# Kernel optimization log

Hardware: AMD Instinct MI355X
Metric: run time of the kernel (lower is better)

## Reference

```python
import jax, jax.numpy as jnp
import numpy as np

DIM = 64   # model dim == d_inner (expand=1)
Hh = 64
Ww = 64
BATCH = 4
D_IN = 64
N_ST = 8   # d_state
DT_R = 4   # dt_rank = ceil(dim/16)
K = 4      # depthwise conv kernel
NB = 8     # total CrossMambaBlocks: 4 (depth=1) + 4 final cross blocks


def setup_inputs():
    key = jax.random.key(0)
    ks = iter(jax.random.split(key, 40))
    def rn(shape, s=0.02):
        return jax.random.normal(next(ks), shape, jnp.float32) * s
    A_init = jnp.log(jnp.tile(jnp.arange(1, N_ST + 1, dtype=jnp.float32), (NB, D_IN, 1)))
    return dict(
        img1=rn((BATCH, DIM, Hh, Ww), 1.0), img2=rn((BATCH, DIM, Hh, Ww), 1.0),
        img1_sum=rn((BATCH, DIM, Hh, Ww), 1.0), img2_sum=rn((BATCH, DIM, Hh, Ww), 1.0),
        norm0_w=jnp.ones((NB, DIM)), norm0_b=jnp.zeros((NB, DIM)),
        norm1_w=jnp.ones((NB, DIM)), norm1_b=jnp.zeros((NB, DIM)),
        in_w=rn((NB, 2 * D_IN, DIM)), in_b=jnp.zeros((NB, 2 * D_IN)),
        conv_w_f=rn((NB, D_IN, 1, K), 0.1), conv_b_f=jnp.zeros((NB, D_IN)),
        conv_w_b=rn((NB, D_IN, 1, K), 0.1), conv_b_b=jnp.zeros((NB, D_IN)),
        xproj_w_f=rn((NB, DT_R + 2 * N_ST, D_IN)), xproj_w_b=rn((NB, DT_R + 2 * N_ST, D_IN)),
        dtproj_w_f=rn((NB, D_IN, DT_R), 0.1), dtproj_b_f=jnp.zeros((NB, D_IN)),
        dtproj_w_b=rn((NB, D_IN, DT_R), 0.1), dtproj_b_b=jnp.zeros((NB, D_IN)),
        A_log_f=A_init, A_log_b=A_init,
        D_f=jnp.ones((NB, D_IN)), D_b=jnp.ones((NB, D_IN)),
        ln_w=jnp.ones((NB, D_IN)), ln_b=jnp.zeros((NB, D_IN)),
        mout_w=rn((NB, DIM, D_IN)), mout_b=jnp.zeros((NB, DIM)),
        fop_w=rn((DIM, 2 * DIM)), fop_b=jnp.zeros((DIM,)),
    )


def _ln(x, w, b):
    m = x.mean(-1, keepdims=True)
    v = ((x - m) ** 2).mean(-1, keepdims=True)
    return (x - m) * jax.lax.rsqrt(v + 1e-5) * w + b


def _dwconv(x, w, b):
    # x: [b,L,d], w: [d,1,K] depthwise causal conv along L
    y = jax.lax.conv_general_dilated(
        x.transpose(0, 2, 1), w, (1,), [(K - 1, 0)],
        dimension_numbers=('NCH', 'OIH', 'NCH'),
        feature_group_count=x.shape[-1])
    return y.transpose(0, 2, 1) + b


def _ssm(u, dt, Bm, Cm, A, Dm):
    # u,dt: [b,L,d]; Bm,Cm: [b,L,n]; A: [d,n]; Dm: [d]
    dA = jnp.exp(dt[..., None] * A)                 # [b,L,d,n]
    dBu = (dt * u)[..., None] * Bm[:, :, None, :]   # [b,L,d,n]
    def step(h, xs):
        dA_t, dBu_t, C_t = xs
        h = dA_t * h + dBu_t
        return h, jnp.einsum('bdn,bn->bd', h, C_t)
    h0 = jnp.zeros(u.shape[:1] + A.shape, u.dtype)
    _, ys = jax.lax.scan(step, h0, (jnp.moveaxis(dA, 1, 0), jnp.moveaxis(dBu, 1, 0), jnp.moveaxis(Cm, 1, 0)))
    return jnp.moveaxis(ys, 0, 1) + u * Dm


def _direction(x_in, extra, conv_w, conv_b, xproj_w, dtproj_w, dtproj_b, A_log, Dm, flip):
    if flip:
        x_in = x_in[:, ::-1]
        extra = extra[:, ::-1]
    u = jax.nn.silu(_dwconv(x_in, conv_w, conv_b))
    dbl = jnp.einsum('bld,ed->ble', extra, xproj_w)     # cross: dt/B/C from extra embedding
    dtr = dbl[..., :DT_R]
    Bm = dbl[..., DT_R:DT_R + N_ST]
    Cm = dbl[..., DT_R + N_ST:]
    dt = jax.nn.softplus(jnp.einsum('blr,dr->bld', dtr, dtproj_w) + dtproj_b)
    y = _ssm(u, dt, Bm, Cm, -jnp.exp(A_log), Dm)
    if flip:
        y = y[:, ::-1]
    return y


def _cross_block(i, x, extra, p):
    skip = x
    x = _ln(x, p['norm0_w'][i], p['norm0_b'][i])
    extra = _ln(extra, p['norm1_w'][i], p['norm1_b'][i])
    xz = jnp.einsum('bld,ed->ble', x, p['in_w'][i]) + p['in_b'][i]
    x_in, z = xz[..., :D_IN], xz[..., D_IN:]
    y_f = _direction(x_in, extra, p['conv_w_f'][i], p['conv_b_f'][i], p['xproj_w_f'][i],
                     p['dtproj_w_f'][i], p['dtproj_b_f'][i], p['A_log_f'][i], p['D_f'][i], False)
    y_b = _direction(x_in, extra, p['conv_w_b'][i], p['conv_b_b'][i], p['xproj_w_b'][i],
                     p['dtproj_w_b'][i], p['dtproj_b_b'][i], p['A_log_b'][i], p['D_b'][i], True)
    y = 0.5 * (y_f + y_b)                    # if_devide_out=True
    y = _ln(y, p['ln_w'][i], p['ln_b'][i])   # use_norm=True
    y = y * jax.nn.silu(z)
    out = jnp.einsum('bld,ed->ble', y, p['mout_w'][i]) + p['mout_b'][i]
    return out + skip


def _forward(img1, img2, img1_sum, img2_sum, norm0_w, norm0_b, norm1_w, norm1_b, in_w, in_b,
             conv_w_f, conv_b_f, conv_w_b, conv_b_b, xproj_w_f, xproj_w_b,
             dtproj_w_f, dtproj_b_f, dtproj_w_b, dtproj_b_b, A_log_f, A_log_b,
             D_f, D_b, ln_w, ln_b, mout_w, mout_b, fop_w, fop_b):
    p = dict(norm0_w=norm0_w, norm0_b=norm0_b, norm1_w=norm1_w, norm1_b=norm1_b,
             in_w=in_w, in_b=in_b, conv_w_f=conv_w_f, conv_b_f=conv_b_f,
             conv_w_b=conv_w_b, conv_b_b=conv_b_b, xproj_w_f=xproj_w_f, xproj_w_b=xproj_w_b,
             dtproj_w_f=dtproj_w_f, dtproj_b_f=dtproj_b_f, dtproj_w_b=dtproj_w_b,
             dtproj_b_b=dtproj_b_b, A_log_f=A_log_f, A_log_b=A_log_b, D_f=D_f, D_b=D_b,
             ln_w=ln_w, ln_b=ln_b, mout_w=mout_w, mout_b=mout_b)
    def seq(t):
        b, c, h, w = t.shape
        return t.reshape(b, c, h * w).transpose(0, 2, 1)   # b (h w) c
    s1, s2, s1s, s2s = seq(img1), seq(img2), seq(img1_sum), seq(img2_sum)
    # depth=1 cross-fusion loop
    s1 = _cross_block(0, s1, s1s, p)
    s2 = _cross_block(1, s2, s2s, p)
    s1s = _cross_block(2, s1s, s1, p)
    s2s = _cross_block(3, s2s, s2, p)
    # final cross blocks
    i1l = _cross_block(4, s1, s2, p)
    i1g = _cross_block(5, s1, s2s, p)
    i2l = _cross_block(6, s2, s1, p)
    i2g = _cross_block(7, s2, s1s, p)
    c1 = jnp.concatenate([i1l, i1g], -1)
    c2 = jnp.concatenate([i2l, i2g], -1)
    fusion = jnp.einsum('ble,ce->blc', 0.5 * (c1 + c2), fop_w) + fop_b
    b = img1.shape[0]
    return fusion.transpose(0, 2, 1).reshape(b, DIM, Hh, Ww)


def reference(img1, img2, img1_sum, img2_sum, norm0_w, norm0_b, norm1_w, norm1_b, in_w, in_b,
              conv_w_f, conv_b_f, conv_w_b, conv_b_b, xproj_w_f, xproj_w_b,
              dtproj_w_f, dtproj_b_f, dtproj_w_b, dtproj_b_b, A_log_f, A_log_b,
              D_f, D_b, ln_w, ln_b, mout_w, mout_b, fop_w, fop_b):
    return _forward(img1, img2, img1_sum, img2_sum, norm0_w, norm0_b, norm1_w, norm1_b, in_w, in_b,
                    conv_w_f, conv_b_f, conv_w_b, conv_b_b, xproj_w_f, xproj_w_b,
                    dtproj_w_f, dtproj_b_f, dtproj_w_b, dtproj_b_b, A_log_f, A_log_b,
                    D_f, D_b, ln_w, ln_b, mout_w, mout_b, fop_w, fop_b)
```

## Files before the change

### kernel.cpp

```cpp
#include <hip/hip_runtime.h>
#include <hip/hip_bf16.h>

#define BX 4
#define LX 4096
#define DX 64
#define NX 8
#define TCH 16
#define NCH 256
#define BLD (BX*LX*DX)

typedef unsigned short u16;
typedef __attribute__((ext_vector_type(8))) short v8s;
typedef __attribute__((ext_vector_type(4))) float v4f;

#define L2E 1.44269504088896f
#define LN2 0.69314718055994531f

__device__ __forceinline__ float b2f(u16 u){ return __uint_as_float(((unsigned)u)<<16); }
__device__ __forceinline__ u16 f2b(float f){
  unsigned u = __float_as_uint(f);
  unsigned r = (u + 0x7FFFu + ((u>>16)&1u)) >> 16;
  return (u16)r;
}
__device__ __forceinline__ float siluf(float x){
  return x * __builtin_amdgcn_rcpf(1.f + __builtin_amdgcn_exp2f(-x*L2E));
}
__device__ __forceinline__ float softplusf(float x){
  const float t = __builtin_amdgcn_exp2f(-fabsf(x)*L2E);
  return fmaxf(x, 0.f) + LN2 * __builtin_amdgcn_logf(1.f + t);
}

__device__ __forceinline__ v4f mfma16(v8s a, v8s b, v4f c){
  return __builtin_amdgcn_mfma_f32_16x16x32_bf16(a, b, c, 0, 0, 0);
}
__device__ __forceinline__ void split8(const float* v, v8s& hi, v8s& lo){
  #pragma unroll
  for(int j=0;j<8;j++){
    const short h = (short)f2b(v[j]);
    hi[j] = h;
    lo[j] = (short)f2b(v[j] - b2f((u16)h));
  }
}
__device__ __forceinline__ void afrag(const float* tile, int lane, int k0, v8s& hi, v8s& lo){
  const float* p = tile + (lane&15)*72 + k0 + ((lane>>4)<<3);
  float v[8];
  const float4 a = *(const float4*)(p);
  const float4 b = *(const float4*)(p+4);
  v[0]=a.x; v[1]=a.y; v[2]=a.z; v[3]=a.w;
  v[4]=b.x; v[5]=b.y; v[6]=b.z; v[7]=b.w;
  split8(v, hi, lo);
}

struct Ctx {
  const float *nw0,*nb0,*nw1,*nb1;
  const float *inw,*inb;
  const float *convw,*convb;
  const float *xproj;
  const float *dtw,*dtb;
  const float *A2,*Dp;
  const float *lnw,*lnb;
  const float *moutw,*moutb;
  const float *fopw,*fopb;
  const u16 *wih,*wil,*wxh,*wxl,*wmh,*wml,*wfh,*wfl;
  float *act[4], *outc[4];
  float *xin[4], *zz[4], *dbl[4], *yy[4], *Pp[4], *qq[4], *hin[4];
};

struct BlkDesc { int i; const float* x; const float* e; float* out; int slot; };
struct StageArgs { BlkDesc d[4]; };

struct PrepEnt { const void* src; float* dst; int n; int mode; };
struct PrepAll { PrepEnt a[26]; };

__global__ __launch_bounds__(256) void k_prep(PrepAll pa, const u16* df){
  const bool isbf = (df[0] == 0x3F80u);
  PrepEnt p = pa.a[blockIdx.y];
  int idx = blockIdx.x*256 + threadIdx.x;
  if(idx < p.n){
    float v = isbf ? b2f(((const u16*)p.src)[idx]) : ((const float*)p.src)[idx];
    if(p.mode==2) v = -__expf(v) * L2E;
    p.dst[idx] = v;
  }
}

struct WPrep { const float* src; u16* dh; u16* dl; int E; int KS; int kind; int i; };
struct WPrepAll { WPrep a[25]; };

__global__ __launch_bounds__(64) void k_prepw(WPrepAll wa, const float* xprojbase){
  WPrep p = wa.a[blockIdx.y];
  const int NT = (p.E + 15) >> 4;
  const int idx = blockIdx.x;
  if(idx >= NT*p.KS) return;
  const int ct = idx / p.KS, ks = idx % p.KS;
  const int lane = threadIdx.x;
  const int g  = ct*16 + (lane & 15);
  const int k0 = ks*32 + ((lane>>4)<<3);
  const int K  = p.KS*32;
  bool valid; const float* srcp = nullptr;
  if(p.kind == 1){
    valid = (g < 40);
    if(valid){ const int dir = g/20, e = g - dir*20;
      srcp = xprojbase + ((size_t)(dir*8 + p.i)*20 + e)*64 + k0; }
  } else {
    valid = (g < p.E);
    if(valid) srcp = p.src + (size_t)g*K + k0;
  }
  float v[8];
  #pragma unroll
  for(int j=0;j<8;j++) v[j] = valid ? srcp[j] : 0.f;
  v8s hi, lo; split8(v, hi, lo);
  const size_t o = ((size_t)idx*64 + lane)*8;
  *(v8s*)(p.dh + o) = hi;
  *(v8s*)(p.dl + o) = lo;
}

struct SeqArgs { const void* src[4]; };

__global__ __launch_bounds__(256) void k_seq(SeqArgs s, Ctx c, const u16* df){
  const bool isbf = (df[0] == 0x3F80u);
  __shared__ float ld[64*65];
  const int t = blockIdx.z, b = blockIdx.y, l0 = blockIdx.x*64;
  float* dst = c.act[t];
  const int tx = threadIdx.x, ty = threadIdx.y;
  if(isbf){
    const u16* src = (const u16*)s.src[t];
    #pragma unroll
    for(int k=0;k<16;k++){ int d = k*4+ty; ld[d*65+tx] = b2f(src[(size_t)(b*64+d)*LX + l0+tx]); }
  } else {
    const float* src = (const float*)s.src[t];
    #pragma unroll
    for(int k=0;k<16;k++){ int d = k*4+ty; ld[d*65+tx] = src[(size_t)(b*64+d)*LX + l0+tx]; }
  }
  __syncthreads();
  #pragma unroll
  for(int k=0;k<16;k++){ int p = k*4+ty; dst[(size_t)(b*LX + l0+p)*64 + tx] = ld[tx*65+p]; }
}

__device__ __forceinline__ void coop72(float* sb, const float* g, int t){
  #pragma unroll
  for(int k=0;k<4;k++){
    const int idx = k*256 + t;
    const int row = idx >> 4;
    const int c4  = (idx & 15) << 2;
    *(float4*)(sb + row*72 + c4) = *(const float4*)(g + (size_t)row*64 + c4);
  }
}
__device__ __forceinline__ void coop72_avg(float* sb, const float* g0, const float* g1, int t){
  #pragma unroll
  for(int k=0;k<4;k++){
    const int idx = k*256 + t;
    const int row = idx >> 4;
    const int c4  = (idx & 15) << 2;
    const float4 a = *(const float4*)(g0 + (size_t)row*64 + c4);
    const float4 b = *(const float4*)(g1 + (size_t)row*64 + c4);
    float4 o; o.x=0.5f*(a.x+b.x); o.y=0.5f*(a.y+b.y); o.z=0.5f*(a.z+b.z); o.w=0.5f*(a.w+b.w);
    *(float4*)(sb + row*72 + c4) = o;
  }
}

__device__ __forceinline__ void ln72(float* sb, int lane, const float* w, const float* b){
  float r[64];
  float* p = sb + lane*72;
  #pragma unroll
  for(int cc=0;cc<64;cc+=4){ float4 v = *(const float4*)(p+cc); r[cc]=v.x; r[cc+1]=v.y; r[cc+2]=v.z; r[cc+3]=v.w; }
  float m=0.f;
  #pragma unroll
  for(int d=0;d<64;d++) m += r[d];
  m *= (1.f/64.f);
  float va=0.f;
  #pragma unroll
  for(int d=0;d<64;d++){ float t=r[d]-m; va += t*t; }
  va *= (1.f/64.f);
  const float rs = rsqrtf(va + 1e-5f);
  #pragma unroll
  for(int d=0;d<64;d++) r[d] = (r[d]-m)*rs*w[d] + b[d];
  #pragma unroll
  for(int cc=0;cc<64;cc+=4){ float4 v={r[cc],r[cc+1],r[cc+2],r[cc+3]}; *(float4*)(p+cc)=v; }
}

__global__ __launch_bounds__(256) void k_front(Ctx c, StageArgs sa){
  __shared__ __align__(16) float sx[64*72];
  __shared__ __align__(16) float se[64*72];
  const BlkDesc bd = sa.d[blockIdx.y];
  const int i = bd.i;
  const int tile = blockIdx.x;
  const int b = tile >> 6;
  const int l0 = (tile & 63) << 6;
  const int bl0 = b*LX + l0;
  const int t = threadIdx.x;
  const int wave = t >> 6, lane = t & 63;

  coop72(sx, bd.x + (size_t)bl0*64, t);
  coop72(se, bd.e + (size_t)bl0*64, t);
  __syncthreads();
  if(wave == 0)      ln72(sx, lane, c.nw0 + i*64, c.nb0 + i*64);
  else if(wave == 1) ln72(se, lane, c.nw1 + i*64, c.nb1 + i*64);
  __syncthreads();

  const int m0 = wave*16;
  const int q  = lane >> 4;
  const int n15 = lane & 15;

  {
    v8s ah[2], al[2];
    afrag(sx + m0*72, lane, 0,  ah[0], al[0]);
    afrag(sx + m0*72, lane, 32, ah[1], al[1]);
    const v8s* WH = (const v8s*)c.wih + (size_t)i*1024;
    const v8s* WL = (const v8s*)c.wil + (size_t)i*1024;
    #pragma unroll 1
    for(int ct=0; ct<8; ct++){
      const int colg = ct*16 + n15;
      const float bias = c.inb[i*128 + colg];
      v4f acc = {bias, bias, bias, bias};
      #pragma unroll
      for(int ks=0; ks<2; ks++){
        const v8s wh = WH[(ct*2+ks)*64 + lane];
        const v8s wl = WL[(ct*2+ks)*64 + lane];
        acc = mfma16(ah[ks], wl, acc);
        acc = mfma16(al[ks], wh, acc);
        acc = mfma16(ah[ks], wh, acc);
      }
      float* baseo = (colg < 64) ? c.xin[bd.slot] : c.zz[bd.slot];
      const int col = colg & 63;
      #pragma unroll
      for(int r=0;r<4;r++){
        const int row = m0 + q*4 + r;
        baseo[(size_t)(bl0+row)*64 + col] = acc[r];
      }
    }
  }
  {
    v8s ah[2], al[2];
    afrag(se + m0*72, lane, 0,  ah[0], al[0]);
    afrag(se + m0*72, lane, 32, ah[1], al[1]);
    const v8s* WH = (const v8s*)c.wxh + (size_t)i*384;
    const v8s* WL = (const v8s*)c.wxl + (size_t)i*384;
    #pragma unroll 1
    for(int ct=0; ct<3; ct++){
      v4f acc = {0.f,0.f,0.f,0.f};
      #pragma unroll
      for(int ks=0; ks<2; ks++){
        const v8s wh = WH[(ct*2+ks)*64 + lane];
        const v8s wl = WL[(ct*2+ks)*64 + lane];
        acc = mfma16(ah[ks], wl, acc);
        acc = mfma16(al[ks], wh, acc);
        acc = mfma16(ah[ks], wh, acc);
      }
      const int g = ct*16 + n15;
      if(g < 40){
        const int dir = (g >= 20);
        const int e = g - dir*20;
        float* dp = c.dbl[bd.slot] + (size_t)dir*((size_t)BX*LX*20);
        #pragma unroll
        for(int r=0;r<4;r++){
          const int row = m0 + q*4 + r;
          dp[(size_t)(bl0+row)*20 + e] = acc[r];
        }
      }
    }
  }
}

template<int PASS>
__device__ __forceinline__ void scan_body(const Ctx& c, const StageArgs& sa){
  __shared__ float meta[TCH*20];
  const int zid = blockIdx.z;
  const int j = zid >> 1, dir = zid & 1;
  const BlkDesc bd = sa.d[j];
  const int i = bd.i, slot = bd.slot;
  const int ch = blockIdx.x, b = blockIdx.y;
  const int d = threadIdx.x;
  const int pb = (dir*8 + i)*64 + d;

  const float4 cwv = *(const float4*)(c.convw + (size_t)pb*4);
  const float  cbv = c.convb[pb];
  const float4 dwv = *(const float4*)(c.dtw + (size_t)pb*4);
  const float  dtbv = c.dtb[pb];
  const float4 A2a = *(const float4*)(c.A2 + (size_t)pb*8);
  const float4 A2b = *(const float4*)(c.A2 + (size_t)pb*8 + 4);
  float A2[8] = {A2a.x,A2a.y,A2a.z,A2a.w,A2b.x,A2b.y,A2b.z,A2b.w};

  {
    const float4* s = (const float4*)(c.dbl[slot] + (size_t)dir*((size_t)BX*LX*20)
                                      + (size_t)(b*LX + ch*TCH)*20);
    float4* dst = (float4*)meta;
    #pragma unroll
    for(int k=0;k<2;k++){ int idx = k*64 + d; if(idx < 80) dst[idx] = s[idx]; }
  }
  __syncthreads();

  const float* X = c.xin[slot] + (size_t)b*LX*64 + d;
  float h[8];
  if(PASS==1){
    #pragma unroll
    for(int n=0;n<8;n++) h[n]=0.f;
  } else {
    const float* hp = c.hin[slot] + (size_t)(dir*NCH + ch)*((size_t)BX*512) + (size_t)b*512 + d;
    #pragma unroll
    for(int n=0;n<8;n++) h[n] = hp[n*64];
  }
  const float Dv = (PASS==3) ? c.Dp[pb] : 0.f;
  float* Y = (PASS==3) ? (c.yy[slot] + (size_t)(dir*BX + b)*LX*64 + d) : (float*)0;

  int lbase, sgn;
  if(dir==0){ lbase = ch*TCH;          sgn =  1; }
  else      { lbase = ch*TCH + TCH-1;  sgn = -1; }
  float w0,w1,w2;
  { int p0 = lbase - 3*sgn; w0 = (p0>=0 && p0<LX)? X[(size_t)p0*64] : 0.f; }
  { int p1 = lbase - 2*sgn; w1 = (p1>=0 && p1<LX)? X[(size_t)p1*64] : 0.f; }
  { int p2 = lbase - 1*sgn; w2 = (p2>=0 && p2<LX)? X[(size_t)p2*64] : 0.f; }

  const float* Xp = X + (size_t)lbase*64;
  float* Yp = (PASS==3) ? (Y + (size_t)lbase*64) : (float*)0;
  const float* mp = meta + (dir ? (TCH-1)*20 : 0);
  const int xstep = sgn*64;
  const int mstep = sgn*20;

  float S = 0.f;
  #pragma unroll 4
  for(int t=0;t<TCH;t++){
    const float xc = *Xp;
    const float u = siluf(cwv.x*w0 + cwv.y*w1 + cwv.z*w2 + cwv.w*xc + cbv);
    const float4 m0  = *(const float4*)(mp);
    const float4 mb0 = *(const float4*)(mp+4);
    const float4 mb1 = *(const float4*)(mp+8);
    const float dt = softplusf(m0.x*dwv.x + m0.y*dwv.y + m0.z*dwv.z + m0.w*dwv.w + dtbv);
    const float du = dt*u;
    const float Bv[8] = {mb0.x,mb0.y,mb0.z,mb0.w,mb1.x,mb1.y,mb1.z,mb1.w};
    #pragma unroll
    for(int n=0;n<8;n++){
      const float dA = __builtin_amdgcn_exp2f(dt*A2[n]);
      h[n] = dA*h[n] + du*Bv[n];
    }
    if(PASS==3){
      const float4 mc0 = *(const float4*)(mp+12);
      const float4 mc1 = *(const float4*)(mp+16);
      const float Cv[8] = {mc0.x,mc0.y,mc0.z,mc0.w,mc1.x,mc1.y,mc1.z,mc1.w};
      float yv = u*Dv;
      #pragma unroll
      for(int n=0;n<8;n++) yv += h[n]*Cv[n];
      *Yp = yv;
      Yp += xstep;
    } else {
      S += dt;
    }
    w0=w1; w1=w2; w2=xc;
    Xp += xstep; mp += mstep;
  }
  if(PASS==1){
    float* Pw = c.Pp[slot] + (size_t)(dir*NCH + ch)*((size_t)BX*512) + (size_t)b*512 + d;
    float* Qw = c.qq[slot] + (size_t)(dir*NCH + ch)*((size_t)BX*512) + (size_t)b*512 + d;
    #pragma unroll
    for(int n=0;n<8;n++){
      Pw[n*64] = __builtin_amdgcn_exp2f(A2[n]*S);
      Qw[n*64] = h[n];
    }
  }
}

__global__ __launch_bounds__(64) void k_scan1(Ctx c, StageArgs sa){ scan_body<1>(c, sa); }
__global__ __launch_bounds__(64) void k_scan3(Ctx c, StageArgs sa){ scan_body<3>(c, sa); }

__global__ __launch_bounds__(64) void k_mid(Ctx c, StageArgs sa){
  const int b = blockIdx.x >> 3;
  const int seg = blockIdx.x & 7;
  const int dir = blockIdx.y & 1, j = blockIdx.y >> 1;
  const BlkDesc bd = sa.d[j];
  const int slot = bd.slot;
  const int nd = seg*64 + threadIdx.x;
  const size_t base = (size_t)dir*NCH*((size_t)BX*512) + (size_t)b*512 + nd;
  const size_t STR = (size_t)BX*512;
  const float* P = c.Pp[slot] + base;
  const float* Q = c.qq[slot] + base;
  float* H = c.hin[slot] + base;
  float h = 0.f;
  float Pv[16], Qv[16];
  #pragma unroll 1
  for(int g=0; g<NCH/16; g++){
    #pragma unroll
    for(int k=0;k<16;k++){
      const int ch = dir ? (NCH-1 - (g*16+k)) : (g*16+k);
      Pv[k] = P[(size_t)ch*STR]; Qv[k] = Q[(size_t)ch*STR];
    }
    #pragma unroll
    for(int k=0;k<16;k++){
      const int ch = dir ? (NCH-1 - (g*16+k)) : (g*16+k);
      H[(size_t)ch*STR] = h;
      h = fmaf(Pv[k], h, Qv[k]);
    }
  }
}

__global__ __launch_bounds__(256) void k_back(Ctx c, StageArgs sa){
  __shared__ __align__(16) float sy[64*72];
  __shared__ __align__(16) float sz[64*72];
  __shared__ __align__(16) float sk[64*72];
  const BlkDesc bd = sa.d[blockIdx.y];
  const int i = bd.i, slot = bd.slot;
  const int tile = blockIdx.x;
  const int b = tile >> 6;
  const int l0 = (tile & 63) << 6;
  const int bl0 = b*LX + l0;
  const int t = threadIdx.x;
  const int wave = t >> 6, lane = t & 63;

  coop72_avg(sy, c.yy[slot] + (size_t)b*LX*64 + (size_t)l0*64,
                 c.yy[slot] + (size_t)(BX+b)*LX*64 + (size_t)l0*64, t);
  coop72(sz, c.zz[slot] + (size_t)bl0*64, t);
  coop72(sk, bd.x + (size_t)bl0*64, t);
  __syncthreads();
  if(wave == 0){
    ln72(sy, lane, c.lnw + i*64, c.lnb + i*64);
    float* p = sy + lane*72;
    const float* zp = sz + lane*72;
    #pragma unroll
    for(int d=0;d<64;d++){ const float zv = zp[d]; p[d] *= siluf(zv)/(zv==0.f?1.f:zv)*zv; }
  }
  __syncthreads();

  const int m0 = wave*16;
  const int q  = lane >> 4;
  const int n15 = lane & 15;
  v8s ah[2], al[2];
  afrag(sy + m0*72, lane, 0,  ah[0], al[0]);
  afrag(sy + m0*72, lane, 32, ah[1], al[1]);
  const v8s* WH = (const v8s*)c.wmh + (size_t)i*512;
  const v8s* WL = (const v8s*)c.wml + (size_t)i*512;
  #pragma unroll 1
  for(int ct=0; ct<4; ct++){
    const int col = ct*16 + n15;
    const float bias = c.moutb[i*64 + col];
    v4f acc = {bias, bias, bias, bias};
    #pragma unroll
    for(int ks=0; ks<2; ks++){
      const v8s wh = WH[(ct*2+ks)*64 + lane];
      const v8s wl = WL[(ct*2+ks)*64 + lane];
      acc = mfma16(ah[ks], wl, acc);
      acc = mfma16(al[ks], wh, acc);
      acc = mfma16(ah[ks], wh, acc);
    }
    #pragma unroll
    for(int r=0;r<4;r++){
      const int row = m0 + q*4 + r;
      bd.out[(size_t)(bl0+row)*64 + col] = acc[r] + sk[row*72 + col];
    }
  }
}

__global__ __launch_bounds__(256) void k_fusion(Ctx c, void* outp, const u16* df){
  const bool isbf = (df[0] == 0x3F80u);
  __shared__ __align__(16) float sL[64*72];
  __shared__ __align__(16) float sH[64*72];
  __shared__ __align__(16) float sT[64*68];
  const int tile = blockIdx.x;
  const int b = tile >> 6;
  const int l0 = (tile & 63) << 6;
  const int bl0 = b*LX + l0;
  const int t = threadIdx.x;
  const int wave = t >> 6, lane = t & 63;

  coop72_avg(sL, c.outc[0] + (size_t)bl0*64, c.outc[2] + (size_t)bl0*64, t);
  coop72_avg(sH, c.outc[1] + (size_t)bl0*64, c.outc[3] + (size_t)bl0*64, t);
  __syncthreads();

  const int m0 = wave*16;
  const int q  = lane >> 4;
  const int n15 = lane & 15;
  v8s ah[4], al[4];
  afrag(sL + m0*72, lane, 0,  ah[0], al[0]);
  afrag(sL + m0*72, lane, 32, ah[1], al[1]);
  afrag(sH + m0*72, lane, 0,  ah[2], al[2]);
  afrag(sH + m0*72, lane, 32, ah[3], al[3]);
  const v8s* WH = (const v8s*)c.wfh;
  const v8s* WL = (const v8s*)c.wfl;
  #pragma unroll 1
  for(int ct=0; ct<4; ct++){
    const int col = ct*16 + n15;
    const float bias = c.fopb[col];
    v4f acc = {bias, bias, bias, bias};
    #pragma unroll
    for(int ks=0; ks<4; ks++){
      const v8s wh = WH[(ct*4+ks)*64 + lane];
      const v8s wl = WL[(ct*4+ks)*64 + lane];
      acc = mfma16(ah[ks], wl, acc);
      acc = mfma16(al[ks], wh, acc);
      acc = mfma16(ah[ks], wh, acc);
    }
    #pragma unroll
    for(int r=0;r<4;r++) sT[col*68 + m0 + q*4 + r] = acc[r];
  }
  __syncthreads();

  const int o  = t >> 2;
  const int p0 = (t & 3) * 16;
  float v[16];
  #pragma unroll
  for(int k=0;k<16;k+=4){
    const float4 x = *(const float4*)(sT + o*68 + p0 + k);
    v[k]=x.x; v[k+1]=x.y; v[k+2]=x.z; v[k+3]=x.w;
  }
  const size_t off = (size_t)(b*64+o)*LX + l0 + p0;
  if(isbf){
    u16 hb[16];
    #pragma unroll
    for(int k=0;k<16;k++) hb[k] = f2b(v[k]);
    uint4 u0, u1;
    u0.x = hb[0] | ((unsigned)hb[1]<<16);  u0.y = hb[2] | ((unsigned)hb[3]<<16);
    u0.z = hb[4] | ((unsigned)hb[5]<<16);  u0.w = hb[6] | ((unsigned)hb[7]<<16);
    u1.x = hb[8] | ((unsigned)hb[9]<<16);  u1.y = hb[10]| ((unsigned)hb[11]<<16);
    u1.z = hb[12]| ((unsigned)hb[13]<<16); u1.w = hb[14]| ((unsigned)hb[15]<<16);
    *(uint4*)((u16*)outp + off)     = u0;
    *(uint4*)((u16*)outp + off + 8) = u1;
  } else {
    float* fo = (float*)outp + off;
    #pragma unroll
    for(int k=0;k<16;k+=4){ float4 x={v[k],v[k+1],v[k+2],v[k+3]}; *(float4*)(fo+k)=x; }
  }
}

extern "C" void kernel_launch(void* const* d_in, const int* in_sizes, int n_in,
                              void* d_out, int out_size, void* d_ws, size_t ws_size,
                              hipStream_t stream){
  (void)in_sizes; (void)out_size;
  if(n_in < 30) return;
  const u16* df = (const u16*)d_in[22];
  float* w = (float*)d_ws;
  size_t off = 0;
  auto al = [&](size_t n){ float* p = w + off; off += n; return p; };

  Ctx c;
  float* nw0 = al(512);  float* nb0 = al(512);
  float* nw1 = al(512);  float* nb1 = al(512);
  float* inw = al(65536); float* inb = al(1024);
  float* convw = al(4096); float* convb = al(1024);
  float* xproj = al(20480);
  float* dtw = al(4096); float* dtb = al(1024);
  float* A2 = al(8192);  float* Dp = al(1024);
  float* lnw = al(512);  float* lnb = al(512);
  float* moutw = al(32768); float* moutb = al(512);
  float* fopw = al(8192); float* fopb = al(64);
  c.nw0=nw0; c.nb0=nb0; c.nw1=nw1; c.nb1=nb1;
  c.inw=inw; c.inb=inb; c.convw=convw; c.convb=convb;
  c.xproj=xproj; c.dtw=dtw; c.dtb=dtb; c.A2=A2; c.Dp=Dp;
  c.lnw=lnw; c.lnb=lnb; c.moutw=moutw; c.moutb=moutb; c.fopw=fopw; c.fopb=fopb;

  u16* wih = (u16*)al(32768); u16* wil = (u16*)al(32768);
  u16* wxh = (u16*)al(12288); u16* wxl = (u16*)al(12288);
  u16* wmh = (u16*)al(16384); u16* wml = (u16*)al(16384);
  u16* wfh = (u16*)al(4096);  u16* wfl = (u16*)al(4096);
  c.wih=wih; c.wil=wil; c.wxh=wxh; c.wxl=wxl; c.wmh=wmh; c.wml=wml; c.wfh=wfh; c.wfl=wfl;

  for(int k=0;k<4;k++) c.act[k]  = al(BLD);
  for(int k=0;k<4;k++) c.outc[k] = al(BLD);

  const size_t CHW = 2*(size_t)NCH*BX*512;
  const size_t SLOT = (size_t)BLD + BLD + 2*(size_t)BX*LX*20 + 2*(size_t)BLD + 3*CHW;
  const size_t avail = ws_size/4;
  int nslots = 4;
  while(nslots>1 && off + (size_t)nslots*SLOT > avail) nslots >>= 1;
  for(int s=0;s<nslots;s++){
    c.xin[s]=al(BLD); c.zz[s]=al(BLD); c.dbl[s]=al(2*(size_t)BX*LX*20);
    c.yy[s]=al(2*(size_t)BLD);
    c.Pp[s]=al(CHW); c.qq[s]=al(CHW); c.hin[s]=al(CHW);
  }
  for(int s=nslots;s<4;s++){
    c.xin[s]=c.xin[0]; c.zz[s]=c.zz[0]; c.dbl[s]=c.dbl[0]; c.yy[s]=c.yy[0];
    c.Pp[s]=c.Pp[0]; c.qq[s]=c.qq[0]; c.hin[s]=c.hin[0];
  }

  PrepAll pa;
  int kk = 0;
  auto add = [&](int idx, float* dst, int n, int mode){
    pa.a[kk].src=d_in[idx]; pa.a[kk].dst=dst; pa.a[kk].n=n; pa.a[kk].mode=mode; kk++;
  };
  add(4,  nw0, 512, 0); add(5,  nb0, 512, 0);
  add(6,  nw1, 512, 0); add(7,  nb1, 512, 0);
  add(8,  inw, 65536, 0); add(9, inb, 1024, 0);
  add(10, convw, 2048, 0);      add(11, convb, 512, 0);
  add(12, convw+2048, 2048, 0); add(13, convb+512, 512, 0);
  add(14, xproj, 10240, 0);     add(15, xproj+10240, 10240, 0);
  add(16, dtw, 2048, 0);        add(17, dtb, 512, 0);
  add(18, dtw+2048, 2048, 0);   add(19, dtb+512, 512, 0);
  add(20, A2, 4096, 2);         add(21, A2+4096, 4096, 2);
  add(22, Dp, 512, 0);          add(23, Dp+512, 512, 0);
  add(24, lnw, 512, 0);         add(25, lnb, 512, 0);
  add(26, moutw, 32768, 0);     add(27, moutb, 512, 0);
  add(28, fopw, 8192, 0);       add(29, fopb, 64, 0);
  k_prep<<<dim3(256,26),256,0,stream>>>(pa, df);

  WPrepAll wa;
  for(int i=0;i<8;i++) wa.a[i]    = { inw + (size_t)i*8192,  wih + (size_t)i*8192, wil + (size_t)i*8192, 128, 2, 0, i };
  for(int i=0;i<8;i++) wa.a[8+i]  = { nullptr,               wxh + (size_t)i*3072, wxl + (size_t)i*3072,  48, 2, 1, i };
  for(int i=0;i<8;i++) wa.a[16+i] = { moutw + (size_t)i*4096, wmh + (size_t)i*4096, wml + (size_t)i*4096, 64, 2, 0, i };
  wa.a[24] = { fopw, wfh, wfl, 64, 4, 0, 0 };
  k_prepw<<<dim3(16,25),64,0,stream>>>(wa, xproj);

  SeqArgs sq;
  for(int t=0;t<4;t++) sq.src[t] = d_in[t];
  k_seq<<<dim3(64,BX,4), dim3(64,4), 0, stream>>>(sq, c, df);

  BlkDesc SA[2] = {{0, c.act[0], c.act[2], c.act[0], 0},
                   {1, c.act[1], c.act[3], c.act[1], 0}};
  BlkDesc SB[2] = {{2, c.act[2], c.act[0], c.act[2], 0},
                   {3, c.act[3], c.act[1], c.act[3], 0}};
  BlkDesc SC[4] = {{4, c.act[0], c.act[1], c.outc[0], 0},
                   {5, c.act[0], c.act[3], c.outc[1], 0},
                   {6, c.act[1], c.act[0], c.outc[2], 0},
                   {7, c.act[1], c.act[2], c.outc[3], 0}};

  auto run = [&](BlkDesc* ds, int cnt){
    for(int k=0;k<cnt;k+=nslots){
      int n = cnt-k; if(n>nslots) n = nslots;
      StageArgs sa;
      for(int j=0;j<n;j++){ sa.d[j] = ds[k+j]; sa.d[j].slot = j; }
      for(int j=n;j<4;j++) sa.d[j] = sa.d[0];
      k_front<<<dim3(256,n),      256, 0, stream>>>(c, sa);
      k_scan1<<<dim3(NCH,BX,2*n),  64, 0, stream>>>(c, sa);
      k_mid  <<<dim3(BX*8,2*n),    64, 0, stream>>>(c, sa);
      k_scan3<<<dim3(NCH,BX,2*n),  64, 0, stream>>>(c, sa);
      k_back <<<dim3(256,n),      256, 0, stream>>>(c, sa);
    }
  };
  run(SA,2); run(SB,2); run(SC,4);
  k_fusion<<<256,256,0,stream>>>(c, d_out, df);
}
```

Baseline: 387.1 us.

## Merge weight prep kernels, rebalance block stages, widen mid-scan unroll, simplify gating

The scalar-parameter conversion and the hi/lo bf16 weight splitting now run in a single launch. The split now reads the original inputs directly, so the intermediate fp32 copies of the in, x-proj, out and fusion weights are no longer made. The block schedule is regrouped so two of the final cross blocks run alongside blocks 2 and 3, giving stages of 2, 4 and 2 blocks. The mid-chunk carry scan loads 32 chunks per batch instead of 16, and the SiLU gating expression is reduced to a plain multiply. Together these aim to cut launch count, prep traffic and some per-element arithmetic. The cost is a more complex prep kernel and higher register use in the mid scan.

```diff
diff --git a/kernel.cpp b/kernel.cpp
--- a/kernel.cpp
+++ b/kernel.cpp
@@ -53,14 +53,13 @@
 
 struct Ctx {
   const float *nw0,*nb0,*nw1,*nb1;
-  const float *inw,*inb;
+  const float *inb;
   const float *convw,*convb;
-  const float *xproj;
   const float *dtw,*dtb;
   const float *A2,*Dp;
   const float *lnw,*lnb;
-  const float *moutw,*moutb;
-  const float *fopw,*fopb;
+  const float *moutb;
+  const float *fopb;
   const u16 *wih,*wil,*wxh,*wxl,*wmh,*wml,*wfh,*wfl;
   float *act[4], *outc[4];
   float *xin[4], *zz[4], *dbl[4], *yy[4], *Pp[4], *qq[4], *hin[4];
@@ -70,48 +69,52 @@
 struct StageArgs { BlkDesc d[4]; };
 
 struct PrepEnt { const void* src; float* dst; int n; int mode; };
-struct PrepAll { PrepEnt a[26]; };
-
-__global__ __launch_bounds__(256) void k_prep(PrepAll pa, const u16* df){
+struct PrepAll { PrepEnt a[21]; };
+struct WPrep { const void* sA; const void* sB; u16* dh; u16* dl; long off; int E; int KS; int kind; int i; };
+struct WPrepAll { WPrep a[25]; };
+
+__global__ __launch_bounds__(256) void k_prep(PrepAll pa, WPrepAll wa, const u16* df){
   const bool isbf = (df[0] == 0x3F80u);
-  PrepEnt p = pa.a[blockIdx.y];
-  int idx = blockIdx.x*256 + threadIdx.x;
-  if(idx < p.n){
-    float v = isbf ? b2f(((const u16*)p.src)[idx]) : ((const float*)p.src)[idx];
-    if(p.mode==2) v = -__expf(v) * L2E;
-    p.dst[idx] = v;
-  }
-}
-
-struct WPrep { const float* src; u16* dh; u16* dl; int E; int KS; int kind; int i; };
-struct WPrepAll { WPrep a[25]; };
-
-__global__ __launch_bounds__(64) void k_prepw(WPrepAll wa, const float* xprojbase){
-  WPrep p = wa.a[blockIdx.y];
-  const int NT = (p.E + 15) >> 4;
-  const int idx = blockIdx.x;
-  if(idx >= NT*p.KS) return;
-  const int ct = idx / p.KS, ks = idx % p.KS;
-  const int lane = threadIdx.x;
-  const int g  = ct*16 + (lane & 15);
-  const int k0 = ks*32 + ((lane>>4)<<3);
-  const int K  = p.KS*32;
-  bool valid; const float* srcp = nullptr;
-  if(p.kind == 1){
-    valid = (g < 40);
-    if(valid){ const int dir = g/20, e = g - dir*20;
-      srcp = xprojbase + ((size_t)(dir*8 + p.i)*20 + e)*64 + k0; }
+  if(blockIdx.y < 21){
+    PrepEnt p = pa.a[blockIdx.y];
+    int idx = blockIdx.x*256 + threadIdx.x;
+    if(idx < p.n){
+      float v = isbf ? b2f(((const u16*)p.src)[idx]) : ((const float*)p.src)[idx];
+      if(p.mode==2) v = -__expf(v) * L2E;
+      p.dst[idx] = v;
+    }
   } else {
-    valid = (g < p.E);
-    if(valid) srcp = p.src + (size_t)g*K + k0;
-  }
-  float v[8];
-  #pragma unroll
-  for(int j=0;j<8;j++) v[j] = valid ? srcp[j] : 0.f;
-  v8s hi, lo; split8(v, hi, lo);
-  const size_t o = ((size_t)idx*64 + lane)*8;
-  *(v8s*)(p.dh + o) = hi;
-  *(v8s*)(p.dl + o) = lo;
+    WPrep p = wa.a[blockIdx.y - 21];
+    const int wv = threadIdx.x >> 6, lane = threadIdx.x & 63;
+    const int idx = blockIdx.x*4 + wv;
+    const int NT = (p.E + 15) >> 4;
+    if(idx >= NT*p.KS) return;
+    const int ct = idx / p.KS, ks = idx % p.KS;
+    const int g  = ct*16 + (lane & 15);
+    const int k0 = ks*32 + ((lane>>4)<<3);
+    const int K  = p.KS*32;
+    bool valid; long si = 0; const void* sp = p.sA;
+    if(p.kind == 1){
+      valid = (g < 40);
+      const int dir = g/20, e = g - dir*20;
+      if(dir) sp = p.sB;
+      si = ((long)p.i*20 + e)*64 + k0;
+    } else {
+      valid = (g < p.E);
+      si = p.off + (long)g*K + k0;
+    }
+    float v[8];
+    #pragma unroll
+    for(int j2=0;j2<8;j2++){
+      float x = 0.f;
+      if(valid) x = isbf ? b2f(((const u16*)sp)[si+j2]) : ((const float*)sp)[si+j2];
+      v[j2] = x;
+    }
+    v8s hi, lo; split8(v, hi, lo);
+    const size_t o = ((size_t)idx*64 + lane)*8;
+    *(v8s*)(p.dh + o) = hi;
+    *(v8s*)(p.dl + o) = lo;
+  }
 }
 
 struct SeqArgs { const void* src[4]; };
@@ -263,7 +266,7 @@
 
 template<int PASS>
 __device__ __forceinline__ void scan_body(const Ctx& c, const StageArgs& sa){
-  __shared__ float meta[TCH*20];
+  __shared__ __align__(16) float meta[TCH*20];
   const int zid = blockIdx.z;
   const int j = zid >> 1, dir = zid & 1;
   const BlkDesc bd = sa.d[j];
@@ -374,17 +377,17 @@
   const float* Q = c.qq[slot] + base;
   float* H = c.hin[slot] + base;
   float h = 0.f;
-  float Pv[16], Qv[16];
+  float Pv[32], Qv[32];
   #pragma unroll 1
-  for(int g=0; g<NCH/16; g++){
-    #pragma unroll
-    for(int k=0;k<16;k++){
-      const int ch = dir ? (NCH-1 - (g*16+k)) : (g*16+k);
+  for(int g=0; g<NCH/32; g++){
+    #pragma unroll
+    for(int k=0;k<32;k++){
+      const int ch = dir ? (NCH-1 - (g*32+k)) : (g*32+k);
       Pv[k] = P[(size_t)ch*STR]; Qv[k] = Q[(size_t)ch*STR];
     }
     #pragma unroll
-    for(int k=0;k<16;k++){
-      const int ch = dir ? (NCH-1 - (g*16+k)) : (g*16+k);
+    for(int k=0;k<32;k++){
+      const int ch = dir ? (NCH-1 - (g*32+k)) : (g*32+k);
       H[(size_t)ch*STR] = h;
       h = fmaf(Pv[k], h, Qv[k]);
     }
@@ -414,7 +417,7 @@
     float* p = sy + lane*72;
     const float* zp = sz + lane*72;
     #pragma unroll
-    for(int d=0;d<64;d++){ const float zv = zp[d]; p[d] *= siluf(zv)/(zv==0.f?1.f:zv)*zv; }
+    for(int d=0;d<64;d++){ p[d] *= siluf(zp[d]); }
   }
   __syncthreads();
 
@@ -531,18 +534,17 @@
   Ctx c;
   float* nw0 = al(512);  float* nb0 = al(512);
   float* nw1 = al(512);  float* nb1 = al(512);
-  float* inw = al(65536); float* inb = al(1024);
+  float* inb = al(1024);
   float* convw = al(4096); float* convb = al(1024);
-  float* xproj = al(20480);
   float* dtw = al(4096); float* dtb = al(1024);
   float* A2 = al(8192);  float* Dp = al(1024);
   float* lnw = al(512);  float* lnb = al(512);
-  float* moutw = al(32768); float* moutb = al(512);
-  float* fopw = al(8192); float* fopb = al(64);
+  float* moutb = al(512);
+  float* fopb = al(64);
   c.nw0=nw0; c.nb0=nb0; c.nw1=nw1; c.nb1=nb1;
-  c.inw=inw; c.inb=inb; c.convw=convw; c.convb=convb;
-  c.xproj=xproj; c.dtw=dtw; c.dtb=dtb; c.A2=A2; c.Dp=Dp;
-  c.lnw=lnw; c.lnb=lnb; c.moutw=moutw; c.moutb=moutb; c.fopw=fopw; c.fopb=fopb;
+  c.inb=inb; c.convw=convw; c.convb=convb;
+  c.dtw=dtw; c.dtb=dtb; c.A2=A2; c.Dp=Dp;
+  c.lnw=lnw; c.lnb=lnb; c.moutb=moutb; c.fopb=fopb;
 
   u16* wih = (u16*)al(32768); u16* wil = (u16*)al(32768);
   u16* wxh = (u16*)al(12288); u16* wxl = (u16*)al(12288);
@@ -575,37 +577,36 @@
   };
   add(4,  nw0, 512, 0); add(5,  nb0, 512, 0);
   add(6,  nw1, 512, 0); add(7,  nb1, 512, 0);
-  add(8,  inw, 65536, 0); add(9, inb, 1024, 0);
+  add(9,  inb, 1024, 0);
   add(10, convw, 2048, 0);      add(11, convb, 512, 0);
   add(12, convw+2048, 2048, 0); add(13, convb+512, 512, 0);
-  add(14, xproj, 10240, 0);     add(15, xproj+10240, 10240, 0);
   add(16, dtw, 2048, 0);        add(17, dtb, 512, 0);
   add(18, dtw+2048, 2048, 0);   add(19, dtb+512, 512, 0);
   add(20, A2, 4096, 2);         add(21, A2+4096, 4096, 2);
   add(22, Dp, 512, 0);          add(23, Dp+512, 512, 0);
   add(24, lnw, 512, 0);         add(25, lnb, 512, 0);
-  add(26, moutw, 32768, 0);     add(27, moutb, 512, 0);
-  add(28, fopw, 8192, 0);       add(29, fopb, 64, 0);
-  k_prep<<<dim3(256,26),256,0,stream>>>(pa, df);
+  add(27, moutb, 512, 0);
+  add(29, fopb, 64, 0);
 
   WPrepAll wa;
-  for(int i=0;i<8;i++) wa.a[i]    = { inw + (size_t)i*8192,  wih + (size_t)i*8192, wil + (size_t)i*8192, 128, 2, 0, i };
-  for(int i=0;i<8;i++) wa.a[8+i]  = { nullptr,               wxh + (size_t)i*3072, wxl + (size_t)i*3072,  48, 2, 1, i };
-  for(int i=0;i<8;i++) wa.a[16+i] = { moutw + (size_t)i*4096, wmh + (size_t)i*4096, wml + (size_t)i*4096, 64, 2, 0, i };
-  wa.a[24] = { fopw, wfh, wfl, 64, 4, 0, 0 };
-  k_prepw<<<dim3(16,25),64,0,stream>>>(wa, xproj);
+  for(int i=0;i<8;i++) wa.a[i]    = { d_in[8],  nullptr,  wih+(size_t)i*8192, wil+(size_t)i*8192, (long)i*8192, 128, 2, 0, i };
+  for(int i=0;i<8;i++) wa.a[8+i]  = { d_in[14], d_in[15], wxh+(size_t)i*3072, wxl+(size_t)i*3072, 0,            48, 2, 1, i };
+  for(int i=0;i<8;i++) wa.a[16+i] = { d_in[26], nullptr,  wmh+(size_t)i*4096, wml+(size_t)i*4096, (long)i*4096, 64, 2, 0, i };
+  wa.a[24] = { d_in[28], nullptr, wfh, wfl, 0, 64, 4, 0, 0 };
+
+  k_prep<<<dim3(16,46),256,0,stream>>>(pa, wa, df);
 
   SeqArgs sq;
   for(int t=0;t<4;t++) sq.src[t] = d_in[t];
   k_seq<<<dim3(64,BX,4), dim3(64,4), 0, stream>>>(sq, c, df);
 
-  BlkDesc SA[2] = {{0, c.act[0], c.act[2], c.act[0], 0},
+  BlkDesc R1[2] = {{0, c.act[0], c.act[2], c.act[0], 0},
                    {1, c.act[1], c.act[3], c.act[1], 0}};
-  BlkDesc SB[2] = {{2, c.act[2], c.act[0], c.act[2], 0},
-                   {3, c.act[3], c.act[1], c.act[3], 0}};
-  BlkDesc SC[4] = {{4, c.act[0], c.act[1], c.outc[0], 0},
-                   {5, c.act[0], c.act[3], c.outc[1], 0},
-                   {6, c.act[1], c.act[0], c.outc[2], 0},
+  BlkDesc R2[4] = {{2, c.act[2], c.act[0], c.act[2], 0},
+                   {3, c.act[3], c.act[1], c.act[3], 0},
+                   {4, c.act[0], c.act[1], c.outc[0], 0},
+                   {6, c.act[1], c.act[0], c.outc[2], 0}};
+  BlkDesc R3[2] = {{5, c.act[0], c.act[3], c.outc[1], 0},
                    {7, c.act[1], c.act[2], c.outc[3], 0}};
 
   auto run = [&](BlkDesc* ds, int cnt){
@@ -621,6 +622,6 @@
       k_back <<<dim3(256,n),      256, 0, stream>>>(c, sa);
     }
   };
-  run(SA,2); run(SB,2); run(SC,4);
+  run(R1,2); run(R2,4); run(R3,2);
   k_fusion<<<256,256,0,stream>>>(c, d_out, df);
 }
```

New measurement: 376.5 us. -2.7%, faster.
